# Optimization experiments

Measured on AMD Instinct MI355X. Metric: run time of the kernel, lower is better.

The kernel has to match this reference:

```python
import jax, jax.numpy as jnp
import numpy as np
from jax import lax

DN_CONV = ('NCHW', 'OIHW', 'NCHW')
DN_DECONV = ('NCHW', 'IOHW', 'NCHW')


def _conv(x, w, b, stride, pad):
    y = lax.conv_general_dilated(x, w, (stride, stride), ((pad, pad), (pad, pad)),
                                 dimension_numbers=DN_CONV)
    return y + b[None, :, None, None]


def _deconv(x, w, b):
    # torch ConvTranspose2d(k=4, stride=2, padding=1): equivalent to conv with
    # lhs_dilation=2, padding=k-1-p=2, spatially flipped kernel, weight [Cin,Cout,kH,kW].
    wf = w[:, :, ::-1, ::-1]
    y = lax.conv_general_dilated(x, wf, (1, 1), ((2, 2), (2, 2)),
                                 lhs_dilation=(2, 2), dimension_numbers=DN_DECONV)
    return y + b[None, :, None, None]


def setup_inputs() -> dict:
    key = jax.random.key(0)
    ks = jax.random.split(key, 14)
    s = 0.05
    H, D, K = 128, 64, 512  # hidden, embedding_dim, num_embeddings
    inp = {
        'x': jax.random.normal(ks[0], (32, 3, 256, 256), jnp.float32),
        'enc_w1': jax.random.normal(ks[1], (H, 3, 4, 4), jnp.float32) * s,
        'enc_b1': jnp.zeros((H,), jnp.float32),
        'enc_w2': jax.random.normal(ks[2], (H, H, 4, 4), jnp.float32) * s,
        'enc_b2': jnp.zeros((H,), jnp.float32),
        'enc_w3': jax.random.normal(ks[3], (D, H, 3, 3), jnp.float32) * s,
        'enc_b3': jnp.zeros((D,), jnp.float32),
        'codebook': jax.random.uniform(ks[4], (K, D), jnp.float32, -1.0 / K, 1.0 / K),
        'dec_w1': jax.random.normal(ks[5], (H, D, 3, 3), jnp.float32) * s,
        'dec_b1': jnp.zeros((H,), jnp.float32),
        'dec_w2': jax.random.normal(ks[6], (H, H, 4, 4), jnp.float32) * s,  # [Cin,Cout,4,4]
        'dec_b2': jnp.zeros((H,), jnp.float32),
        'dec_w3': jax.random.normal(ks[7], (H, 3, 4, 4), jnp.float32) * s,  # [Cin,Cout,4,4]
        'dec_b3': jnp.zeros((3,), jnp.float32),
    }
    return inp


def reference(x, enc_w1, enc_b1, enc_w2, enc_b2, enc_w3, enc_b3, codebook,
              dec_w1, dec_b1, dec_w2, dec_b2, dec_w3, dec_b3):
    # encoder
    h = jax.nn.relu(_conv(x, enc_w1, enc_b1, 2, 1))
    h = jax.nn.relu(_conv(h, enc_w2, enc_b2, 2, 1))
    z_e = _conv(h, enc_w3, enc_b3, 1, 1)  # [B, D, 64, 64]

    # vector quantization (faithful to torch .view(-1, D) memory reshape)
    D = codebook.shape[1]
    flat = z_e.reshape(-1, D)  # [N, D]
    d2 = (jnp.sum(flat * flat, axis=1, keepdims=True)
          + jnp.sum(codebook * codebook, axis=1)
          - 2.0 * flat @ codebook.T)  # [N, K]
    idx = jnp.argmin(d2, axis=1)
    z_q = jnp.take(codebook, idx, axis=0).reshape(z_e.shape)

    # decoder
    h = jax.nn.relu(_conv(z_q, dec_w1, dec_b1, 1, 1))
    h = jax.nn.relu(_deconv(h, dec_w2, dec_b2))
    x_recon = _deconv(h, dec_w3, dec_b3)
    return (x_recon, z_e, z_q)
```

## Files before the change

kernel.cpp:

```cpp
#include <hip/hip_runtime.h>
#include <hip/hip_bf16.h>


typedef unsigned short u16;
typedef unsigned int u32;
typedef unsigned long long u64;
typedef __attribute__((ext_vector_type(8))) short short8;
typedef __attribute__((ext_vector_type(4))) float f32x4;

__device__ __forceinline__ float bf2f(u16 u) {
    union { u32 i; float f; } x; x.i = ((u32)u) << 16; return x.f;
}
__device__ __forceinline__ u16 f2bf(float f) {
    __hip_bfloat16 h = __float2bfloat16(f);
    return *reinterpret_cast<u16*>(&h);
}

__global__ void g_k3(const float* __restrict__ w, u16* __restrict__ wg,
                     int CIN, int COUT)
{
    int idx = blockIdx.x * 256 + threadIdx.x;
    if (idx >= 9 * CIN * COUT) return;
    int ci = idx % CIN;
    int co = (idx / CIN) % COUT;
    int s  = idx / (CIN * COUT);
    wg[idx] = f2bf(w[(co * CIN + ci) * 9 + s]);
}

__global__ void g_enc2(const float* __restrict__ w, u16* __restrict__ wg)
{
    int idx = blockIdx.x * 256 + threadIdx.x;
    int ci = idx & 127, co = (idx >> 7) & 127, s = (idx >> 14) & 3, p = idx >> 16;
    int a = p >> 1, b = p & 1, j = s >> 1, i = s & 1;
    int ky = (1 - a) + 2 * j, kx = (1 - b) + 2 * i;
    wg[idx] = f2bf(w[((co << 7 | ci) << 4) + ky * 4 + kx]);
}

__global__ void g_dec2(const float* __restrict__ w, u16* __restrict__ wg)
{
    int idx = blockIdx.x * 256 + threadIdx.x;
    int ci = idx & 127, co = (idx >> 7) & 127, s = (idx >> 14) & 3, p = idx >> 16;
    int py = p >> 1, px = p & 1, j = s >> 1, i = s & 1;
    wg[idx] = f2bf(w[((ci << 7 | co) << 4) + (3 - (py + 2 * j)) * 4 + (3 - (px + 2 * i))]);
}

__global__ void g_dec3m(const float* __restrict__ w, u16* __restrict__ wg)
{
    int idx = blockIdx.x * 256 + threadIdx.x;
    if (idx >= 18432) return;
    int ci  = idx & 127;
    int row = (idx >> 7) & 15;
    int t   = idx >> 11;
    int dy = t / 3 - 1, dx = t % 3 - 1;
    float v = 0.f;
    if (row < 12) {
        int p = row / 3, co = row % 3;
        int py = p >> 1, px = p & 1;
        int a = dy + 1 - py, b2 = dx + 1 - px;
        if (a >= 0 && a <= 1 && b2 >= 0 && b2 <= 1)
            v = w[((ci * 3 + co) * 4 + (3 - (py + 2 * a))) * 4 + (3 - (px + 2 * b2))];
    }
    wg[idx] = f2bf(v);
}

__global__ void g_enc1(const float* __restrict__ w, u16* __restrict__ wg)
{
    int idx = blockIdx.x * 256 + threadIdx.x;
    if (idx >= 8192) return;
    int ci = idx & 3, kx = (idx >> 2) & 3, ky = (idx >> 4) & 3, co = idx >> 6;
    float v = 0.f;
    if (ci < 3) v = w[((co * 3 + ci) * 4 + ky) * 4 + kx];
    wg[idx] = f2bf(v);
}

__global__ void g_cbk(const float* __restrict__ cbk, u16* __restrict__ cb,
                      float* __restrict__ cn)
{
    int idx = blockIdx.x * 256 + threadIdx.x;
    if (idx >= 32768) return;
    cb[idx] = f2bf(cbk[idx]);
    if (idx < 512) {
        float s = 0.f;
        const float* r = cbk + idx * 64;
        for (int i = 0; i < 64; i++) s += r[i] * r[i];
        cn[idx] = s;
    }
}

__global__ __launch_bounds__(256) void xcl_k(
    const float* __restrict__ x, u16* __restrict__ xcl)
{
    const int y = blockIdx.x % 258, n = blockIdx.x / 258;
    const int gy = y - 1;
    for (int xx = threadIdx.x; xx < 258; xx += 256) {
        const int gx = xx - 1;
        u16 pk[4] = {0, 0, 0, 0};
        if (gy >= 0 && gy < 256 && gx >= 0 && gx < 256) {
            const size_t base = ((size_t)n * 3 * 256 + gy) * 256 + gx;
            pk[0] = f2bf(x[base]);
            pk[1] = f2bf(x[base + 65536]);
            pk[2] = f2bf(x[base + 131072]);
        }
        *(u64*)(xcl + ((size_t)(n * 258 + y) * 258 + xx) * 4) = *(const u64*)pk;
    }
}

__global__ __launch_bounds__(256) void enc1m_k(
    const u16* __restrict__ xcl, const u16* __restrict__ wg,
    const float* __restrict__ bias, u16* __restrict__ P)
{
    const int tid = threadIdx.x;
    const int l = tid & 63, w = tid >> 6;
    const int ln = l & 15, kg = l >> 4;
    const int px = w >> 1, half = w & 1;

    const int oy = blockIdx.x & 127;
    const int n  = blockIdx.x >> 7;
    const int p  = (oy & 1) * 2 + px;
    const int yy = oy >> 1;

    short8 af[8][2];
#pragma unroll
    for (int u = 0; u < 8; u++)
#pragma unroll
        for (int s = 0; s < 2; s++)
            af[u][s] = *(const short8*)(wg + ((u * 16 + ln) << 6) + s * 32 + 8 * kg);

    const u16* xn = xcl + (size_t)n * 258 * 258 * 4;
    const int r0 = 2 * oy;

#pragma unroll
    for (int t = 0; t < 2; t++) {
        const int xq = half * 32 + t * 16 + ln;
        const int ox = px + 2 * xq;

        short8 bf[2];
#pragma unroll
        for (int s = 0; s < 2; s++) {
            const int row = r0 + 2 * s + (kg >> 1);
            bf[s] = *(const short8*)(xn + ((size_t)row * 258 + 2 * ox) * 4
                                     + (kg & 1) * 8);
        }

        f32x4 acc[8];
#pragma unroll
        for (int u = 0; u < 8; u++) acc[u] = (f32x4){0.f, 0.f, 0.f, 0.f};
#pragma unroll
        for (int u = 0; u < 8; u++) {
            acc[u] = __builtin_amdgcn_mfma_f32_16x16x32_bf16(af[u][0], bf[0], acc[u], 0, 0, 0);
            acc[u] = __builtin_amdgcn_mfma_f32_16x16x32_bf16(af[u][1], bf[1], acc[u], 0, 0, 0);
        }

#pragma unroll
        for (int u = 0; u < 8; u++) {
            const int cobase = u * 16 + 4 * kg;
            u16 pk[4];
#pragma unroll
            for (int r = 0; r < 4; r++)
                pk[r] = f2bf(fmaxf(acc[u][r] + bias[cobase + r], 0.f));
            *(u64*)(P + ((((size_t)(n * 4 + p) * 64 + yy) * 64 + xq) << 7) + cobase)
                = *(const u64*)pk;
        }
    }
}

template<int J, int I, int NP, int NCW, int CI, int OUTM>
__global__ __launch_bounds__(512) void conv_mx3(
    const u16* __restrict__ x, const u16* __restrict__ wg,
    const float* __restrict__ bias, void* __restrict__ yv,
    int COUT)
{
    constexpr int G = 8 / NCW;
    constexpr int RS = 2 * G + 2;
    constexpr int TASKS = RS * 68 * 4;
    constexpr int SLOTS = (TASKS + 511) / 512;
    constexpr int CHP = CI / 32;
    constexpr int NCHUNK = NP * CHP;
    __shared__ u16 XL[RS * 68 * 40];

    const int tid = threadIdx.x;
    const int l = tid & 63, wv = tid >> 6;
    const int kg = l >> 4, ln = l & 15;
    const int cw = wv % NCW, g = wv / NCW;

    int b = blockIdx.x;
    constexpr int TILES = 64 / (2 * G);
    const int tile = b % TILES;  b /= TILES;
    const int n = b;
    const int OY0 = tile * (2 * G);

    bool valid[SLOTS], okm[SLOTS];
    int goff[SLOTS], loff[SLOTS];
#pragma unroll
    for (int s = 0; s < SLOTS; s++) {
        const int idx = s * 512 + tid;
        valid[s] = idx < TASKS;
        const int q = idx & 3, cc = (idx >> 2) % 68, r = (idx >> 2) / 68;
        const int gr = OY0 - 1 + r, gx = cc - 1;
        okm[s] = valid[s] && gr >= 0 && gr < 64 && gx >= 0 && gx < 64;
        goff[s] = okm[s] ? ((gr * 64 + gx) * CI + 8 * q) : 0;
        loff[s] = (r * 68 + cc) * 40 + 8 * q;
    }

    f32x4 acc[2][8];
#pragma unroll
    for (int u = 0; u < 2; u++)
#pragma unroll
        for (int t = 0; t < 8; t++) acc[u][t] = (f32x4){0.f, 0.f, 0.f, 0.f};

    const u16* xn = x + (size_t)n * NP * CI * 4096;
    const int co0 = cw * 32 + ln;
    const short8 z8 = (short8){0, 0, 0, 0, 0, 0, 0, 0};

    short8 pf[SLOTS];
    {
        const u16* xp = xn;
#pragma unroll
        for (int s = 0; s < SLOTS; s++)
            pf[s] = okm[s] ? *(const short8*)(xp + goff[s]) : z8;
    }

    for (int c = 0; c < NCHUNK; c++) {
        __syncthreads();
#pragma unroll
        for (int s = 0; s < SLOTS; s++)
            if (valid[s]) *(short8*)(XL + loff[s]) = pf[s];
        __syncthreads();

        if (c + 1 < NCHUNK) {
            const int cn_ = c + 1;
            const u16* xp = xn + (size_t)(cn_ / CHP) * CI * 4096
                            + (cn_ % CHP) * 32;
#pragma unroll
            for (int s = 0; s < SLOTS; s++)
                pf[s] = okm[s] ? *(const short8*)(xp + goff[s]) : z8;
        }

        const int p = c / CHP;
        const int ci0 = (c % CHP) * 32;
        int dy0, dx0;
        const u16* wgp;
        if (NP == 4) {
            dy0 = -(p >> 1); dx0 = -(p & 1);
            wgp = wg + (size_t)p * J * I * COUT * CI;
        } else {
            dy0 = -1; dx0 = -1; wgp = wg;
        }

#define TAP_ROW(jv)                                                          \
        {                                                                    \
            short8 wf0[I], wf1[I];                                           \
            _Pragma("unroll")                                                \
            for (int i = 0; i < I; i++) {                                    \
                const size_t wb = ((size_t)((jv) * I + i) * COUT + co0)      \
                                  * CI + ci0 + 8 * kg;                       \
                wf0[i] = *(const short8*)(wgp + wb);                         \
                wf1[i] = *(const short8*)(wgp + wb + (size_t)16 * CI);       \
            }                                                                \
            _Pragma("unroll")                                                \
            for (int i = 0; i < I; i++) {                                    \
                _Pragma("unroll")                                            \
                for (int t = 0; t < 8; t++) {                                \
                    const int rf = (t >> 2) + 2 * g + dy0 + 1 + (jv);        \
                    const int cf = (t & 3) * 16 + ln + dx0 + 1 + i;          \
                    const short8 bf = *(const short8*)(                      \
                        XL + (rf * 68 + cf) * 40 + 8 * kg);                  \
                    acc[0][t] = __builtin_amdgcn_mfma_f32_16x16x32_bf16(     \
                        wf0[i], bf, acc[0][t], 0, 0, 0);                     \
                    acc[1][t] = __builtin_amdgcn_mfma_f32_16x16x32_bf16(     \
                        wf1[i], bf, acc[1][t], 0, 0, 0);                     \
                }                                                            \
            }                                                                \
        }

        if constexpr (J == 2) {
            TAP_ROW(0); TAP_ROW(1);
        } else {
            TAP_ROW(0); TAP_ROW(1); TAP_ROW(2);
        }
#undef TAP_ROW
    }

#pragma unroll
    for (int u = 0; u < 2; u++) {
        const int cob = cw * 32 + u * 16 + 4 * kg;
#pragma unroll
        for (int t = 0; t < 8; t++) {
            const int oy = OY0 + 2 * g + (t >> 2);
            const int ox = (t & 3) * 16 + ln;
            if constexpr (OUTM == 1) {
                float* out = (float*)yv;
#pragma unroll
                for (int rr = 0; rr < 4; rr++)
                    out[(((size_t)n * COUT + cob + rr) * 64 + oy) * 64 + ox]
                        = acc[u][t][rr] + bias[cob + rr];
            } else {
                u16 pk[4];
#pragma unroll
                for (int rr = 0; rr < 4; rr++)
                    pk[rr] = f2bf(fmaxf(acc[u][t][rr] + bias[cob + rr], 0.f));
                *(u64*)((u16*)yv + ((size_t)(n * 64 + oy) * 64 + ox) * COUT
                        + cob) = *(const u64*)pk;
            }
        }
    }
}

__global__ __launch_bounds__(512) void dec2f_k(
    const u16* __restrict__ x, const u16* __restrict__ wg,
    const float* __restrict__ bias, u16* __restrict__ y)
{
    constexpr int RS = 4;
    constexpr int TASKS = RS * 68 * 4;
    constexpr int SLOTS = 3;
    __shared__ u16 XL[RS * 68 * 40];

    const int tid = threadIdx.x;
    const int l = tid & 63, wv = tid >> 6;
    const int kg = l >> 4, ln = l & 15;
    const int cw = wv & 3, ch = wv >> 2;

    int b = blockIdx.x;
    const int tile = b & 31;  b >>= 5;
    const int n = b;
    const int OY0 = tile * 2;

    bool valid[SLOTS], okm[SLOTS];
    int goff[SLOTS], loff[SLOTS];
#pragma unroll
    for (int s = 0; s < SLOTS; s++) {
        const int idx = s * 512 + tid;
        valid[s] = idx < TASKS;
        const int q = idx & 3, cc = (idx >> 2) % 68, r = (idx >> 2) / 68;
        const int gr = OY0 - 1 + r, gx = cc - 1;
        okm[s] = valid[s] && gr >= 0 && gr < 64 && gx >= 0 && gx < 64;
        goff[s] = okm[s] ? ((gr * 64 + gx) * 128 + 8 * q) : 0;
        loff[s] = (r * 68 + cc) * 40 + 8 * q;
    }

    f32x4 acc[4][2][4];
#pragma unroll
    for (int pc = 0; pc < 4; pc++)
#pragma unroll
        for (int u = 0; u < 2; u++)
#pragma unroll
            for (int t = 0; t < 4; t++) acc[pc][u][t] = (f32x4){0.f, 0.f, 0.f, 0.f};

    const u16* xn = x + (size_t)n * 64 * 64 * 128;
    const int co0 = cw * 32 + ln;
    const short8 z8 = (short8){0, 0, 0, 0, 0, 0, 0, 0};

    short8 pf[SLOTS];
#pragma unroll
    for (int s = 0; s < SLOTS; s++)
        pf[s] = okm[s] ? *(const short8*)(xn + goff[s]) : z8;

    for (int c = 0; c < 4; c++) {
        __syncthreads();
#pragma unroll
        for (int s = 0; s < SLOTS; s++)
            if (valid[s]) *(short8*)(XL + loff[s]) = pf[s];
        __syncthreads();

        if (c < 3) {
            const u16* xp = xn + (c + 1) * 32;
#pragma unroll
            for (int s = 0; s < SLOTS; s++)
                pf[s] = okm[s] ? *(const short8*)(xp + goff[s]) : z8;
        }

        const int ci0 = c * 32;
#pragma unroll
        for (int pc = 0; pc < 4; pc++) {
            const int dy0 = (pc >> 1) - 1, dx0 = (pc & 1) - 1;
            const u16* wgp = wg + (size_t)pc * 4 * 128 * 128;
            short8 wf0[4], wf1[4];
#pragma unroll
            for (int s4 = 0; s4 < 4; s4++) {
                const size_t wb = ((size_t)s4 * 128 + co0) * 128 + ci0 + 8 * kg;
                wf0[s4] = *(const short8*)(wgp + wb);
                wf1[s4] = *(const short8*)(wgp + wb + (size_t)16 * 128);
            }
#pragma unroll
            for (int t = 0; t < 4; t++) {
                const int m = t >> 1;
                const int cbase = ch * 32 + (t & 1) * 16 + ln;
#pragma unroll
                for (int j = 0; j < 2; j++)
#pragma unroll
                    for (int i = 0; i < 2; i++) {
                        const int rf = m + dy0 + 1 + j;
                        const int cf = cbase + dx0 + 1 + i;
                        const short8 bf = *(const short8*)(
                            XL + (rf * 68 + cf) * 40 + 8 * kg);
                        acc[pc][0][t] = __builtin_amdgcn_mfma_f32_16x16x32_bf16(
                            wf0[j * 2 + i], bf, acc[pc][0][t], 0, 0, 0);
                        acc[pc][1][t] = __builtin_amdgcn_mfma_f32_16x16x32_bf16(
                            wf1[j * 2 + i], bf, acc[pc][1][t], 0, 0, 0);
                    }
            }
        }
    }

#pragma unroll
    for (int pc = 0; pc < 4; pc++)
#pragma unroll
        for (int u = 0; u < 2; u++) {
            const int cob = cw * 32 + u * 16 + 4 * kg;
#pragma unroll
            for (int t = 0; t < 4; t++) {
                const int oy = OY0 + (t >> 1);
                const int ox = ch * 32 + (t & 1) * 16 + ln;
                const int OY = 2 * oy + (pc >> 1), OX = 2 * ox + (pc & 1);
                u16 pk[4];
#pragma unroll
                for (int rr = 0; rr < 4; rr++)
                    pk[rr] = f2bf(fmaxf(acc[pc][u][t][rr] + bias[cob + rr], 0.f));
                *(u64*)(y + ((size_t)(n * 128 + OY) * 128 + OX) * 128 + cob)
                    = *(const u64*)pk;
            }
        }
}

__global__ __launch_bounds__(256) void dec3m_k(
    const u16* __restrict__ A2, const u16* __restrict__ wg,
    const float* __restrict__ bias, float* __restrict__ out)
{
    const int tid = threadIdx.x;
    const int l = tid & 63, wvi = tid >> 6;
    const int ln = l & 15, kg = l >> 4;

    int b = blockIdx.x;
    const int mxT = b & 7;  b >>= 3;
    const int myT = b & 3;  b >>= 2;
    const int n = b;
    const int X0 = mxT * 16;
    const int MY0 = myT * 32 + wvi * 8;
    const int xx = X0 + ln;

    const short8 z8 = (short8){0, 0, 0, 0, 0, 0, 0, 0};

    f32x4 acc[8];
#pragma unroll
    for (int m = 0; m < 8; m++) acc[m] = (f32x4){0.f, 0.f, 0.f, 0.f};

    int xoff[3]; bool xok[3];
#pragma unroll
    for (int sh = 0; sh < 3; sh++) {
        const int xv = xx + sh - 1;
        xok[sh] = (xv >= 0) & (xv < 128);
        xoff[sh] = (xok[sh] ? xv : 0) << 7;
    }

    for (int ks = 0; ks < 4; ks++) {
        const int cio = ks * 32 + 8 * kg;

        short8 at[9];
#pragma unroll
        for (int t = 0; t < 9; t++)
            at[t] = *(const short8*)(wg + (((size_t)t * 16 + ln) << 7) + cio);

        short8 B[10][3];
#pragma unroll
        for (int r = 0; r < 10; r++) {
            const int yy = MY0 - 1 + r;
            const bool yok = (yy >= 0) & (yy < 128);
            const size_t rowb = ((size_t)(n * 128 + (yok ? yy : 0)) << 7 << 7);
#pragma unroll
            for (int sh = 0; sh < 3; sh++) {
                short8 v = *(const short8*)(A2 + rowb + xoff[sh] + cio);
                B[r][sh] = (yok & xok[sh]) ? v : z8;
            }
            if (r >= 2) {
                const int m = r - 2;
#pragma unroll
                for (int rr = 0; rr < 3; rr++)
#pragma unroll
                    for (int sh = 0; sh < 3; sh++)
                        acc[m] = __builtin_amdgcn_mfma_f32_16x16x32_bf16(
                            at[rr * 3 + sh], B[m + rr][sh], acc[m], 0, 0, 0);
            }
        }
    }

    if (kg < 3) {
#pragma unroll
        for (int m = 0; m < 8; m++) {
            const int my = MY0 + m;
#pragma unroll
            for (int rr = 0; rr < 4; rr++) {
                const int row = 4 * kg + rr;
                const int p = row / 3, co = row % 3;
                const int oy = 2 * my + (p >> 1);
                const int ox = 2 * xx + (p & 1);
                out[(((size_t)(n * 3 + co)) << 16) + oy * 256 + ox]
                    = acc[m][rr] + bias[co];
            }
        }
    }
}

__global__ __launch_bounds__(256) void vqm2_k(
    const float* __restrict__ ze, const u16* __restrict__ cb,
    const float* __restrict__ cn, const float* __restrict__ cbk,
    float* __restrict__ zq, u16* __restrict__ zqcl)
{
    __shared__ float CN[512];
    __shared__ int IDX[64];
    __shared__ u16 CLDS[64][66];
    const int tid = threadIdx.x;
    const int l = tid & 63, wvi = tid >> 6;
    const int ln = l & 15, kg = l >> 4;

    const int n = blockIdx.x >> 6, y = blockIdx.x & 63;

    for (int i = tid; i < 512; i += 256) CN[i] = cn[i];
    __syncthreads();

    short8 az[2];
#pragma unroll
    for (int ks = 0; ks < 2; ks++) {
        const float* zp = ze + ((size_t)(n * 64 + wvi * 16 + ln) * 64 + y) * 64
                          + ks * 32 + 8 * kg;
        short8 t;
#pragma unroll
        for (int j = 0; j < 8; j++) t[j] = (short)f2bf(zp[j]);
        az[ks] = t;
    }

    float bval[4] = {3.4e38f, 3.4e38f, 3.4e38f, 3.4e38f};
    int bidx[4] = {0, 0, 0, 0};
    for (int nt = 0; nt < 32; nt++) {
        const int code = nt * 16 + ln;
        const short8 b0 = *(const short8*)(cb + (size_t)code * 64 + 8 * kg);
        const short8 b1 = *(const short8*)(cb + (size_t)code * 64 + 32 + 8 * kg);
        f32x4 d = (f32x4){0.f, 0.f, 0.f, 0.f};
        d = __builtin_amdgcn_mfma_f32_16x16x32_bf16(az[0], b0, d, 0, 0, 0);
        d = __builtin_amdgcn_mfma_f32_16x16x32_bf16(az[1], b1, d, 0, 0, 0);
        const float cnv = CN[code];
#pragma unroll
        for (int r = 0; r < 4; r++) {
            const float dist = cnv - 2.f * d[r];
            if (dist < bval[r]) { bval[r] = dist; bidx[r] = code; }
        }
    }
#pragma unroll
    for (int off = 1; off < 16; off <<= 1) {
#pragma unroll
        for (int r = 0; r < 4; r++) {
            const float ov = __shfl_xor(bval[r], off);
            const int oi = __shfl_xor(bidx[r], off);
            if (ov < bval[r] || (ov == bval[r] && oi < bidx[r])) {
                bval[r] = ov; bidx[r] = oi;
            }
        }
    }
    if (ln == 0) {
#pragma unroll
        for (int r = 0; r < 4; r++) IDX[wvi * 16 + 4 * kg + r] = bidx[r];
    }
    __syncthreads();

    {
        const int ci = tid >> 2, ch4 = tid & 3;
        const int bi = IDX[ci];
        const float4* sp = (const float4*)(cbk + (size_t)bi * 64 + ch4 * 16);
        float4* dp = (float4*)(zq + ((size_t)(n * 64 + ci) * 64 + y) * 64 + ch4 * 16);
#pragma unroll
        for (int q = 0; q < 4; q++) dp[q] = sp[q];
    }

    for (int idx = tid; idx < 4096; idx += 256) {
        const int ci = idx >> 6, xx = idx & 63;
        CLDS[ci][xx] = cb[(size_t)IDX[ci] * 64 + xx];
    }
    __syncthreads();
    for (int idx = tid; idx < 4096; idx += 256) {
        const int xx = idx >> 6, ci = idx & 63;
        zqcl[(((size_t)(n * 64 + y) * 64 + xx) << 6) + ci] = CLDS[ci][xx];
    }
}

extern "C" void kernel_launch(void* const* d_in, const int* in_sizes, int n_in,
                              void* d_out, int out_size, void* d_ws, size_t ws_size,
                              hipStream_t stream)
{
    (void)in_sizes; (void)n_in; (void)out_size; (void)ws_size;

    const float* x   = (const float*)d_in[0];
    const float* ew1 = (const float*)d_in[1];
    const float* eb1 = (const float*)d_in[2];
    const float* ew2 = (const float*)d_in[3];
    const float* eb2 = (const float*)d_in[4];
    const float* ew3 = (const float*)d_in[5];
    const float* eb3 = (const float*)d_in[6];
    const float* cbk = (const float*)d_in[7];
    const float* dw1 = (const float*)d_in[8];
    const float* db1 = (const float*)d_in[9];
    const float* dw2 = (const float*)d_in[10];
    const float* db2 = (const float*)d_in[11];
    const float* dw3 = (const float*)d_in[12];
    const float* db3 = (const float*)d_in[13];

    u16* P    = (u16*)d_ws;
    u16* ZQCL = P;
    u16* A2   = P;
    u16* B = (u16*)((char*)d_ws + 134217728);
    u16* XCL = B;
    u16* Wg2 = (u16*)((char*)d_ws + 167772160);
    u16* Wg3 = Wg2 + 262144;
    u16* Wg4 = Wg3 + 73728;
    u16* Wg5 = Wg4 + 73728;
    u16* Wg6 = Wg5 + 262144;
    u16* CB  = Wg6 + 32768;
    u16* Wg1 = CB + 32768;
    float* CNg = (float*)(Wg1 + 8192);

    float* xr = (float*)d_out;
    float* ze = xr + (size_t)32 * 3 * 256 * 256;
    float* zq = ze + (size_t)32 * 64 * 64 * 64;

    g_enc1<<<32, 256, 0, stream>>>(ew1, Wg1);
    g_enc2<<<1024, 256, 0, stream>>>(ew2, Wg2);
    g_k3<<<288, 256, 0, stream>>>(ew3, Wg3, 128, 64);
    g_k3<<<288, 256, 0, stream>>>(dw1, Wg4, 64, 128);
    g_dec2<<<1024, 256, 0, stream>>>(dw2, Wg5);
    g_dec3m<<<72, 256, 0, stream>>>(dw3, Wg6);
    g_cbk<<<128, 256, 0, stream>>>(cbk, CB, CNg);

    xcl_k<<<32 * 258, 256, 0, stream>>>(x, XCL);
    enc1m_k<<<32 * 128, 256, 0, stream>>>(XCL, Wg1, eb1, P);
    conv_mx3<2, 2, 4, 4, 128, 0><<<32 * 16, 512, 0, stream>>>(P, Wg2, eb2, B, 128);
    conv_mx3<3, 3, 1, 2, 128, 1><<<32 * 8, 512, 0, stream>>>(B, Wg3, eb3, ze, 64);
    vqm2_k<<<2048, 256, 0, stream>>>(ze, CB, CNg, cbk, zq, ZQCL);
    conv_mx3<3, 3, 1, 4, 64, 0><<<32 * 16, 512, 0, stream>>>(ZQCL, Wg4, db1, B, 128);
    dec2f_k<<<1024, 512, 0, stream>>>(B, Wg5, db2, A2);
    dec3m_k<<<1024, 256, 0, stream>>>(A2, Wg6, db3, xr);
}
```

Baseline: 581.1 us.

## Split dec2 deconv waves by output phase instead of output-channel group

```diff
diff --git a/kernel.cpp b/kernel.cpp
--- a/kernel.cpp
+++ b/kernel.cpp
@@ -318,7 +318,8 @@
     const int tid = threadIdx.x;
     const int l = tid & 63, wv = tid >> 6;
     const int kg = l >> 4, ln = l & 15;
-    const int cw = wv & 3, ch = wv >> 2;
+    const int pc = wv & 3, ch = wv >> 2;
+    const int py = pc >> 1, px = pc & 1;
 
     int b = blockIdx.x;
     const int tile = b & 31;  b >>= 5;
@@ -338,17 +339,15 @@
         loff[s] = (r * 68 + cc) * 40 + 8 * q;
     }
 
-    f32x4 acc[4][2][4];
-#pragma unroll
-    for (int pc = 0; pc < 4; pc++)
-#pragma unroll
-        for (int u = 0; u < 2; u++)
-#pragma unroll
-            for (int t = 0; t < 4; t++) acc[pc][u][t] = (f32x4){0.f, 0.f, 0.f, 0.f};
+    f32x4 acc[8][4];
+#pragma unroll
+    for (int u = 0; u < 8; u++)
+#pragma unroll
+        for (int t = 0; t < 4; t++) acc[u][t] = (f32x4){0.f, 0.f, 0.f, 0.f};
 
     const u16* xn = x + (size_t)n * 64 * 64 * 128;
-    const int co0 = cw * 32 + ln;
     const short8 z8 = (short8){0, 0, 0, 0, 0, 0, 0, 0};
+    const u16* wgp = wg + (size_t)pc * 4 * 128 * 128;
 
     short8 pf[SLOTS];
 #pragma unroll
@@ -370,56 +369,59 @@
         }
 
         const int ci0 = c * 32;
-#pragma unroll
-        for (int pc = 0; pc < 4; pc++) {
-            const int dy0 = (pc >> 1) - 1, dx0 = (pc & 1) - 1;
-            const u16* wgp = wg + (size_t)pc * 4 * 128 * 128;
-            short8 wf0[4], wf1[4];
-#pragma unroll
-            for (int s4 = 0; s4 < 4; s4++) {
-                const size_t wb = ((size_t)s4 * 128 + co0) * 128 + ci0 + 8 * kg;
-                wf0[s4] = *(const short8*)(wgp + wb);
-                wf1[s4] = *(const short8*)(wgp + wb + (size_t)16 * 128);
+
+        short8 B3[3][2][2];
+#pragma unroll
+        for (int rw = 0; rw < 3; rw++) {
+            const int rf = py + rw;
+#pragma unroll
+            for (int cb = 0; cb < 2; cb++) {
+                const int cf0 = ch * 32 + cb * 16 + ln + px;
+#pragma unroll
+                for (int sh = 0; sh < 2; sh++)
+                    B3[rw][sh][cb] = *(const short8*)(
+                        XL + (rf * 68 + cf0 + sh) * 40 + 8 * kg);
             }
-#pragma unroll
-            for (int t = 0; t < 4; t++) {
-                const int m = t >> 1;
-                const int cbase = ch * 32 + (t & 1) * 16 + ln;
-#pragma unroll
-                for (int j = 0; j < 2; j++)
-#pragma unroll
-                    for (int i = 0; i < 2; i++) {
-                        const int rf = m + dy0 + 1 + j;
-                        const int cf = cbase + dx0 + 1 + i;
-                        const short8 bf = *(const short8*)(
-                            XL + (rf * 68 + cf) * 40 + 8 * kg);
-                        acc[pc][0][t] = __builtin_amdgcn_mfma_f32_16x16x32_bf16(
-                            wf0[j * 2 + i], bf, acc[pc][0][t], 0, 0, 0);
-                        acc[pc][1][t] = __builtin_amdgcn_mfma_f32_16x16x32_bf16(
-                            wf1[j * 2 + i], bf, acc[pc][1][t], 0, 0, 0);
-                    }
-            }
-        }
-    }
-
-#pragma unroll
-    for (int pc = 0; pc < 4; pc++)
-#pragma unroll
-        for (int u = 0; u < 2; u++) {
-            const int cob = cw * 32 + u * 16 + 4 * kg;
-#pragma unroll
-            for (int t = 0; t < 4; t++) {
-                const int oy = OY0 + (t >> 1);
-                const int ox = ch * 32 + (t & 1) * 16 + ln;
-                const int OY = 2 * oy + (pc >> 1), OX = 2 * ox + (pc & 1);
-                u16 pk[4];
-#pragma unroll
-                for (int rr = 0; rr < 4; rr++)
-                    pk[rr] = f2bf(fmaxf(acc[pc][u][t][rr] + bias[cob + rr], 0.f));
-                *(u64*)(y + ((size_t)(n * 128 + OY) * 128 + OX) * 128 + cob)
-                    = *(const u64*)pk;
-            }
-        }
+        }
+
+#pragma unroll
+        for (int u = 0; u < 8; u++) {
+            short8 wf[4];
+#pragma unroll
+            for (int s4 = 0; s4 < 4; s4++)
+                wf[s4] = *(const short8*)(
+                    wgp + ((size_t)s4 * 128 + u * 16 + ln) * 128 + ci0 + 8 * kg);
+#pragma unroll
+            for (int m = 0; m < 2; m++)
+#pragma unroll
+                for (int cb = 0; cb < 2; cb++)
+#pragma unroll
+                    for (int j = 0; j < 2; j++)
+#pragma unroll
+                        for (int i = 0; i < 2; i++)
+                            acc[u][m * 2 + cb] =
+                                __builtin_amdgcn_mfma_f32_16x16x32_bf16(
+                                    wf[j * 2 + i], B3[m + j][i][cb],
+                                    acc[u][m * 2 + cb], 0, 0, 0);
+        }
+    }
+
+#pragma unroll
+    for (int u = 0; u < 8; u++) {
+        const int cob = u * 16 + 4 * kg;
+#pragma unroll
+        for (int t = 0; t < 4; t++) {
+            const int oy = OY0 + (t >> 1);
+            const int ox = ch * 32 + (t & 1) * 16 + ln;
+            const int OY = 2 * oy + py, OX = 2 * ox + px;
+            u16 pk[4];
+#pragma unroll
+            for (int rr = 0; rr < 4; rr++)
+                pk[rr] = f2bf(fmaxf(acc[u][t][rr] + bias[cob + rr], 0.f));
+            *(u64*)(y + ((size_t)(n * 128 + OY) * 128 + OX) * 128 + cob)
+                = *(const u64*)pk;
+        }
+    }
 }
 
 __global__ __launch_bounds__(256) void dec3m_k(
```

Result: no change. 579.0 us (-0.4%).
